# Performance work log

Measured on AMD Instinct MI355X. Metric: run time of the kernel, lower is better.

Reference implementation:

```python
import jax, jax.numpy as jnp
import numpy as np

E, H, F, N, B = 512, 8, 2048, 1024, 4
HD = E // H


def setup_inputs() -> dict:
    key = jax.random.key(0)
    ks = jax.random.split(key, 20)
    s = 0.02
    return {
        "node_inputs": jax.random.normal(ks[0], (N, B, E), jnp.float32),
        "parent_mask": jax.random.uniform(ks[1], (B, N, N), jnp.float32),
        "hidden": jax.random.bernoulli(ks[2], 0.5, (B, N, N)),
        "pad_mask": jax.random.bernoulli(ks[3], 0.1, (B, N)),
        "Wp": jax.random.normal(ks[4], (H, E), jnp.float32) * s,
        "bp": jnp.zeros((H,), jnp.float32),
        "Wc": jax.random.normal(ks[5], (H, E), jnp.float32) * s,
        "bc": jnp.zeros((H,), jnp.float32),
        "Wqkv": jax.random.normal(ks[6], (3 * E, E), jnp.float32) * s,
        "bqkv": jnp.zeros((3 * E,), jnp.float32),
        "Wo": jax.random.normal(ks[7], (E, E), jnp.float32) * s,
        "bo": jnp.zeros((E,), jnp.float32),
        "W1": jax.random.normal(ks[8], (F, E), jnp.float32) * s,
        "b1": jnp.zeros((F,), jnp.float32),
        "W2": jax.random.normal(ks[9], (E, F), jnp.float32) * s,
        "b2": jnp.zeros((E,), jnp.float32),
        "ln1_g": jnp.ones((E,), jnp.float32),
        "ln1_b": jnp.zeros((E,), jnp.float32),
        "ln2_g": jnp.ones((E,), jnp.float32),
        "ln2_b": jnp.zeros((E,), jnp.float32),
    }


def _layer_norm(x, g, b, eps=1e-5):
    m = jnp.mean(x, axis=-1, keepdims=True)
    v = jnp.mean((x - m) ** 2, axis=-1, keepdims=True)
    return (x - m) * jax.lax.rsqrt(v + eps) * g + b


def reference(node_inputs, parent_mask, hidden, pad_mask, Wp, bp, Wc, bc,
              Wqkv, bqkv, Wo, bo, W1, b1, W2, b2, ln1_g, ln1_b, ln2_g, ln2_b):
    x = node_inputs  # (N, B, E), seq-first like nn.TransformerEncoderLayer
    # parent/child per-head biases: Linear(E->H), permuted to (B, H, N)
    pbias = jnp.transpose(x @ Wp.T + bp, (1, 2, 0))
    cbias = jnp.transpose(x @ Wc.T + bc, (1, 2, 0))
    # additive attention bias (B, H, N, N)
    am = (jnp.swapaxes(parent_mask, 1, 2)[:, None] * pbias[..., None]
          + parent_mask[:, None] * cbias[..., None])
    am = jnp.where(hidden[:, None], -jnp.inf, am)
    # multi-head self-attention
    qkv = x @ Wqkv.T + bqkv  # (N, B, 3E)
    q, k, v = jnp.split(qkv, 3, axis=-1)

    def heads(t):  # (N, B, E) -> (B, H, N, HD)
        return jnp.transpose(t.reshape(N, B, H, HD), (1, 2, 0, 3))

    q, k, v = heads(q), heads(k), heads(v)
    scores = jnp.einsum("bhqd,bhkd->bhqk", q, k) / jnp.sqrt(jnp.float32(HD)) + am
    scores = jnp.where(pad_mask[:, None, None, :], -jnp.inf, scores)
    attn = jax.nn.softmax(scores, axis=-1)
    ctx = jnp.einsum("bhqk,bhkd->bhqd", attn, v)  # (B, H, N, HD)
    ctx = jnp.transpose(ctx, (2, 0, 1, 3)).reshape(N, B, E)
    attn_out = ctx @ Wo.T + bo
    # post-norm transformer encoder layer (dropout=0, relu activation)
    y = _layer_norm(x + attn_out, ln1_g, ln1_b)
    ff = jax.nn.relu(y @ W1.T + b1) @ W2.T + b2
    return _layer_norm(y + ff, ln2_g, ln2_b)
```

## Files before the change

kernel.cpp:

```cpp
#include <hip/hip_runtime.h>
#include <hip/hip_bf16.h>
#include <stdint.h>

using bf16 = __hip_bfloat16;

typedef __bf16 bf16x8 __attribute__((ext_vector_type(8)));
typedef float  f32x4  __attribute__((ext_vector_type(4)));

__device__ __forceinline__ float bflo(uint32_t u) { return __uint_as_float(u << 16); }
__device__ __forceinline__ float bfhi(uint32_t u) { return __uint_as_float(u & 0xffff0000u); }

__device__ __forceinline__ void load8(const bf16* p, float* f) {
  uint4 u = *(const uint4*)p;
  f[0] = bflo(u.x); f[1] = bfhi(u.x);
  f[2] = bflo(u.y); f[3] = bfhi(u.y);
  f[4] = bflo(u.z); f[5] = bfhi(u.z);
  f[6] = bflo(u.w); f[7] = bfhi(u.w);
}
__device__ __forceinline__ void load8(const float* p, float* f) {
  float4 a = *(const float4*)p, b = *(const float4*)(p + 4);
  f[0] = a.x; f[1] = a.y; f[2] = a.z; f[3] = a.w;
  f[4] = b.x; f[5] = b.y; f[6] = b.z; f[7] = b.w;
}
__device__ __forceinline__ void store1(float* o, float v) { *o = v; }
__device__ __forceinline__ void store1(bf16* o, float v) { *o = __float2bfloat16(v); }
__device__ __forceinline__ uint32_t bfbits(float x) {
  bf16 v = __float2bfloat16(x);
  return (uint32_t)*(uint16_t*)&v;
}

typedef const uint32_t __attribute__((address_space(1)))* gp_t;
typedef uint32_t __attribute__((address_space(3)))* lp_t;
__device__ __forceinline__ void gload16(const void* g, void* l) {
  __builtin_amdgcn_global_load_lds((gp_t)g, (lp_t)l, 16, 0, 0);
}

__global__ __launch_bounds__(256)
void prep_mask(const float* __restrict__ pm, const int* __restrict__ hid,
               const int* __restrict__ padm, uint32_t* __restrict__ mout,
               const float* __restrict__ x, const float* __restrict__ Wqkv,
               const float* __restrict__ Wo, const float* __restrict__ W1,
               const float* __restrict__ W2, bf16* __restrict__ xb,
               bf16* __restrict__ wq, bf16* __restrict__ wob,
               bf16* __restrict__ w1b, bf16* __restrict__ w2b,
               const float* __restrict__ bqkv, const float* __restrict__ bp,
               const float* __restrict__ bc, const float* __restrict__ Wp,
               const float* __restrict__ Wc, float* __restrict__ bias_ext)
{
  __shared__ float tileT[128][65];
  const int t = threadIdx.x;
  if (blockIdx.x < 512) {
    const int mb = blockIdx.x;
    const int k0 = (mb & 7) * 128, q0 = ((mb >> 3) & 15) * 64, b = mb >> 7;
    const size_t pb = (size_t)b << 20;
#pragma unroll
    for (int i = 0; i < 32; ++i) {
      int idx = t + i * 256;
      int r = idx >> 6, c = idx & 63;
      tileT[r][c] = pm[pb + (size_t)(k0 + r) * 1024 + q0 + c];
    }
    __syncthreads();
#pragma unroll
    for (int i = 0; i < 32; ++i) {
      int idx = t + i * 256;
      int q = idx >> 7, k = idx & 127;
      size_t src = pb + (size_t)(q0 + q) * 1024 + k0 + k;
      int msk = hid[src] | padm[b * 1024 + k0 + k];
      uint32_t u = 0xFFFFFFFFu;
      if (!msk) u = (bfbits(tileT[k][q]) << 16) | bfbits(pm[src]);
      mout[src] = u;
    }
    return;
  }
  const int blk = blockIdx.x - 512;
  if (blk < 2560) {
    size_t j = ((size_t)blk * 256 + t) * 8;
    const float* s; bf16* o; size_t off;
    if      (j < 2097152) { s = x;    o = xb;  off = j; }
    else if (j < 2883584) { s = Wqkv; o = wq;  off = j - 2097152; }
    else if (j < 3145728) { s = Wo;   o = wob; off = j - 2883584; }
    else if (j < 4194304) { s = W1;   o = w1b; off = j - 3145728; }
    else                  { s = W2;   o = w2b; off = j - 4194304; }
    float f[8];
    load8(s + off, f);
    uint4 u;
    u.x = (bfbits(f[1]) << 16) | bfbits(f[0]);
    u.y = (bfbits(f[3]) << 16) | bfbits(f[2]);
    u.z = (bfbits(f[5]) << 16) | bfbits(f[4]);
    u.w = (bfbits(f[7]) << 16) | bfbits(f[6]);
    *(uint4*)(o + off) = u;
  } else {
    int sb = blk - 2560;
    if (sb < 2) {
      int j = (sb * 256 + t) * 8;
      if (j < 4096) {
        float f[8]; load8(Wp + j, f);
#pragma unroll
        for (int i = 0; i < 8; ++i) wq[(size_t)1536 * 512 + j + i] = __float2bfloat16(f[i]);
      }
    } else if (sb < 4) {
      int j = ((sb - 2) * 256 + t) * 8;
      if (j < 4096) {
        float f[8]; load8(Wc + j, f);
#pragma unroll
        for (int i = 0; i < 8; ++i) wq[(size_t)1544 * 512 + j + i] = __float2bfloat16(f[i]);
      }
    } else {
      int j = t * 8;
#pragma unroll
      for (int i = 0; i < 8; ++i) {
        int cc = j + i;
        if (cc < 1664) {
          float v = 0.f;
          if (cc < 1536) v = bqkv[cc];
          else if (cc < 1544) v = bp[cc - 1536];
          else if (cc < 1552) v = bc[cc - 1544];
          bias_ext[cc] = v;
        }
      }
    }
  }
}

__global__ __launch_bounds__(256)
void qkv_gemm(const bf16* __restrict__ A, const bf16* __restrict__ W,
              const float* __restrict__ bias, bf16* __restrict__ outb,
              float* __restrict__ outf)
{
  __shared__ bf16 As[2][128 * 64];
  __shared__ bf16 Bs[2][128 * 64];
  const int t = threadIdx.x;
  const int lane = t & 63, wave = t >> 6;
  const int m0 = (blockIdx.x / 13) * 128, n0 = (blockIdx.x % 13) * 128;
  const int wr = wave >> 1, wc = wave & 1;
  const int frow = lane & 15, ksel = (lane >> 4) * 8;
  f32x4 acc[16] = {};
  const bf16* Ab = A + (size_t)m0 * 512;
  const bf16* Wb = W + (size_t)n0 * 512;

  const int ibs = wave * 64 + lane;
#define STAGE(buf, k0)                                                        \
  {                                                                           \
    _Pragma("unroll")                                                         \
    for (int i = 0; i < 4; ++i) {                                             \
      int idx = i * 256 + ibs;                                                \
      gload16(Ab + (size_t)(idx >> 3) * 512 + (k0) + (idx & 7) * 8,           \
              &As[buf][(i * 256 + wave * 64) * 8]);                           \
    }                                                                         \
    _Pragma("unroll")                                                         \
    for (int i = 0; i < 4; ++i) {                                             \
      int idx = i * 256 + ibs;                                                \
      gload16(Wb + (size_t)(idx >> 3) * 512 + (k0) + (idx & 7) * 8,           \
              &Bs[buf][(i * 256 + wave * 64) * 8]);                           \
    }                                                                         \
  }

  STAGE(0, 0);
  __syncthreads();
#pragma unroll
  for (int ks = 0; ks < 8; ++ks) {
    const int cur = ks & 1;
    if (ks < 7) STAGE(cur ^ 1, (ks + 1) * 64);
#pragma unroll
    for (int kk = 0; kk < 64; kk += 32) {
      bf16x8 af[4], bf_[4];
#pragma unroll
      for (int mt = 0; mt < 4; ++mt)
        af[mt] = *(const bf16x8*)(&As[cur][(wr * 64 + mt * 16 + frow) * 64 + kk + ksel]);
#pragma unroll
      for (int nt = 0; nt < 4; ++nt)
        bf_[nt] = *(const bf16x8*)(&Bs[cur][(wc * 64 + nt * 16 + frow) * 64 + kk + ksel]);
#pragma unroll
      for (int mt = 0; mt < 4; ++mt)
#pragma unroll
        for (int nt = 0; nt < 4; ++nt)
          acc[mt * 4 + nt] = __builtin_amdgcn_mfma_f32_16x16x32_bf16(
              af[mt], bf_[nt], acc[mt * 4 + nt], 0, 0, 0);
    }
    __syncthreads();
  }
#undef STAGE

  const int rb = (lane >> 4) * 4, cb = lane & 15;
#pragma unroll
  for (int mt = 0; mt < 4; ++mt)
#pragma unroll
    for (int nt = 0; nt < 4; ++nt) {
      f32x4 a = acc[mt * 4 + nt];
#pragma unroll
      for (int r = 0; r < 4; ++r) {
        int row = m0 + wr * 64 + mt * 16 + rb + r;
        int col = n0 + wc * 64 + nt * 16 + cb;
        if (col >= 1552) continue;
        float v = a[r] + bias[col];
        int n = row >> 2, b = row & 3;
        if (col >= 1536) {
          int j = col - 1536;
          int hh = j & 7;
          outf[(j < 8 ? 0 : 32768) + (b * 8 + hh) * 1024 + n] = v;
        } else {
          int which = col >> 9, hh = (col >> 6) & 7, d = col & 63;
          if (which == 0) v *= 0.125f;
          size_t idx;
          if (which == 2)
            idx = (((size_t)(64 + b * 8 + hh)) << 16) + (size_t)d * 1024 + n;
          else
            idx = (((size_t)(which * 32 + b * 8 + hh)) << 16) + (size_t)n * 64 + d;
          outb[idx] = __float2bfloat16(v);
        }
      }
    }
}

template<int MODE, int BN>
__global__ __launch_bounds__(256)
void gemm_bt(const bf16* __restrict__ A, const bf16* __restrict__ W,
             const float* __restrict__ bias, bf16* __restrict__ outb,
             float* __restrict__ outf, int M, int Nout, int K, int kLen)
{
  constexpr int NT = BN / 32;
  __shared__ bf16 As[128 * 64];
  __shared__ bf16 Bs[BN * 64];
  const int t = threadIdx.x, lane = t & 63, wave = t >> 6;
  const int m0 = blockIdx.y * 128, n0 = blockIdx.x * BN;
  const int kOff = blockIdx.z * kLen;
  if (MODE == 3) outf += (size_t)blockIdx.z * M * Nout;
  const int wr = wave >> 1, wc = wave & 1;
  const int frow = lane & 15, ksel = (lane >> 4) * 8;
  f32x4 acc[4 * NT] = {};
  const bf16* Ab = A + (size_t)m0 * K;
  const bf16* Wb = W + (size_t)n0 * K;

  for (int k0 = kOff; k0 < kOff + kLen; k0 += 64) {
    __syncthreads();
#pragma unroll
    for (int i = 0; i < 4; ++i) {
      int ib = i * 256 + wave * 64;
      int idx = ib + lane;
      gload16(Ab + (size_t)(idx >> 3) * K + k0 + (idx & 7) * 8, As + ib * 8);
    }
#pragma unroll
    for (int i = 0; i < BN / 32; ++i) {
      int ib = i * 256 + wave * 64;
      int idx = ib + lane;
      gload16(Wb + (size_t)(idx >> 3) * K + k0 + (idx & 7) * 8, Bs + ib * 8);
    }
    __syncthreads();
#pragma unroll
    for (int kk = 0; kk < 64; kk += 32) {
      bf16x8 af[4], bf_[NT];
#pragma unroll
      for (int mt = 0; mt < 4; ++mt)
        af[mt] = *(const bf16x8*)(As + (wr * 64 + mt * 16 + frow) * 64 + kk + ksel);
#pragma unroll
      for (int nt = 0; nt < NT; ++nt)
        bf_[nt] = *(const bf16x8*)(Bs + (wc * (BN / 2) + nt * 16 + frow) * 64 + kk + ksel);
#pragma unroll
      for (int mt = 0; mt < 4; ++mt)
#pragma unroll
        for (int nt = 0; nt < NT; ++nt)
          acc[mt * NT + nt] = __builtin_amdgcn_mfma_f32_16x16x32_bf16(
              af[mt], bf_[nt], acc[mt * NT + nt], 0, 0, 0);
    }
  }
  const int rb = (lane >> 4) * 4, cb = lane & 15;
#pragma unroll
  for (int mt = 0; mt < 4; ++mt)
#pragma unroll
    for (int nt = 0; nt < NT; ++nt) {
      f32x4 a = acc[mt * NT + nt];
#pragma unroll
      for (int r = 0; r < 4; ++r) {
        int row = m0 + wr * 64 + mt * 16 + rb + r;
        int col = n0 + wc * (BN / 2) + nt * 16 + cb;
        if (MODE == 3) {
          outf[(size_t)row * Nout + col] = a[r];
        } else {
          float v = a[r] + bias[col];
          if (MODE == 1) v = fmaxf(v, 0.f);
          outb[(size_t)row * Nout + col] = __float2bfloat16(v);
        }
      }
    }
}

__global__ __launch_bounds__(256, 2)
void attn_mfma(const bf16* __restrict__ qkv, const float* __restrict__ pbw,
               const float* __restrict__ cbw, const uint32_t* __restrict__ mpk,
               bf16* __restrict__ ctxo)
{
  __shared__ bf16 Kt[128 * 64];
  __shared__ bf16 Vt[64 * 128];
  __shared__ bf16 Ps[4][16][136];
  const int t = threadIdx.x, lane = t & 63, wave = t >> 6;
  const int g = lane >> 4, c = lane & 15;
  const int h = blockIdx.y, b = blockIdx.z;
  const int q0 = blockIdx.x * 64 + wave * 16;
  const size_t bh = (size_t)b * 8 + h;
  const bf16* Qp = qkv + (bh << 16);
  const bf16* Kp = qkv + ((32 + bh) << 16);
  const bf16* Vg = qkv + ((64 + bh) << 16);

  bf16x8 qa0 = *(const bf16x8*)(Qp + (size_t)(q0 + c) * 64 + g * 8);
  bf16x8 qa1 = *(const bf16x8*)(Qp + (size_t)(q0 + c) * 64 + 32 + g * 8);

  const float pbq = pbw[bh * 1024 + q0 + c];
  const float cbq = cbw[bh * 1024 + q0 + c];
  const uint32_t* mrp = mpk + (((size_t)b * 1024 + q0 + c) << 10);

  f32x4 oacc[4] = {{0,0,0,0},{0,0,0,0},{0,0,0,0},{0,0,0,0}};
  float m = -1e30f, l = 0.f;

  for (int kt = 0; kt < 8; ++kt) {
    const int k0 = kt * 128;
    __syncthreads();
#pragma unroll
    for (int i = 0; i < 4; ++i) {
      int ib = i * 256 + wave * 64;
      int idx = ib + lane;
      int r = idx >> 3, p = idx & 7;
      gload16(Kp + (size_t)(k0 + r) * 64 + ((p ^ (r & 7)) * 8), Kt + ib * 8);
    }
#pragma unroll
    for (int i = 0; i < 4; ++i) {
      int ib = i * 256 + wave * 64;
      int idx = ib + lane;
      int d = idx >> 4, p = idx & 15;
      gload16(Vg + (size_t)d * 1024 + k0 + ((p ^ (d & 15)) * 8), Vt + ib * 8);
    }
    uint4 mu[8];
#pragma unroll
    for (int nt = 0; nt < 8; ++nt)
      mu[nt] = *(const uint4*)(mrp + k0 + nt * 16 + 4 * g);
    __syncthreads();
    f32x4 sacc[8];
#pragma unroll
    for (int nt = 0; nt < 8; ++nt) {
      f32x4 z = {0.f,0.f,0.f,0.f};
      int r = nt * 16 + c;
      bf16x8 k0f = *(const bf16x8*)(Kt + r * 64 + (( g      ^ (c & 7)) * 8));
      bf16x8 k1f = *(const bf16x8*)(Kt + r * 64 + (((4 + g) ^ (c & 7)) * 8));
      z = __builtin_amdgcn_mfma_f32_16x16x32_bf16(k0f, qa0, z, 0, 0, 0);
      z = __builtin_amdgcn_mfma_f32_16x16x32_bf16(k1f, qa1, z, 0, 0, 0);
      sacc[nt] = z;
    }
    float mx = -1e30f;
#pragma unroll
    for (int nt = 0; nt < 8; ++nt) {
      uint32_t uu[4] = {mu[nt].x, mu[nt].y, mu[nt].z, mu[nt].w};
#pragma unroll
      for (int r = 0; r < 4; ++r) {
        float s = sacc[nt][r] + bfhi(uu[r]) * pbq + bflo(uu[r]) * cbq;
        s = (uu[r] == 0xFFFFFFFFu) ? -1e30f : s;
        sacc[nt][r] = s;
        mx = fmaxf(mx, s);
      }
    }
    mx = fmaxf(mx, __shfl_xor(mx, 16));
    mx = fmaxf(mx, __shfl_xor(mx, 32));
    const float newm = fmaxf(m, mx);
    const float al = __expf(m - newm);
    float ps = 0.f;
#pragma unroll
    for (int nt = 0; nt < 8; ++nt) {
      float p0 = (sacc[nt][0] <= -1e29f) ? 0.f : __expf(sacc[nt][0] - newm);
      float p1 = (sacc[nt][1] <= -1e29f) ? 0.f : __expf(sacc[nt][1] - newm);
      float p2 = (sacc[nt][2] <= -1e29f) ? 0.f : __expf(sacc[nt][2] - newm);
      float p3 = (sacc[nt][3] <= -1e29f) ? 0.f : __expf(sacc[nt][3] - newm);
      ps += (p0 + p1) + (p2 + p3);
      uint2 w;
      w.x = (bfbits(p1) << 16) | bfbits(p0);
      w.y = (bfbits(p3) << 16) | bfbits(p2);
      *(uint2*)&Ps[wave][c][nt * 16 + 4 * g] = w;
    }
    ps += __shfl_xor(ps, 16);
    ps += __shfl_xor(ps, 32);
    l = l * al + ps;
    m = newm;
#pragma unroll
    for (int dt = 0; dt < 4; ++dt) {
      oacc[dt][0] *= al; oacc[dt][1] *= al;
      oacc[dt][2] *= al; oacc[dt][3] *= al;
    }
#pragma unroll
    for (int dt = 0; dt < 4; ++dt) {
      int row = dt * 16 + c;
#pragma unroll
      for (int kc = 0; kc < 4; ++kc) {
        bf16x8 vf = *(const bf16x8*)(Vt + row * 128 + (((kc * 4 + g) ^ c) * 8));
        bf16x8 pf = *(const bf16x8*)&Ps[wave][c][kc * 32 + g * 8];
        oacc[dt] = __builtin_amdgcn_mfma_f32_16x16x32_bf16(vf, pf, oacc[dt], 0, 0, 0);
      }
    }
  }
  const int qg = q0 + c;
  const float inv = (l > 0.f) ? 1.f / l : 0.f;
  bf16* out = ctxo + ((size_t)qg * 4 + b) * 512 + h * 64;
#pragma unroll
  for (int dt = 0; dt < 4; ++dt) {
    uint2 w;
    w.x = (bfbits(oacc[dt][1] * inv) << 16) | bfbits(oacc[dt][0] * inv);
    w.y = (bfbits(oacc[dt][3] * inv) << 16) | bfbits(oacc[dt][2] * inv);
    *(uint2*)(out + dt * 16 + 4 * g) = w;
  }
}

template<typename TA, typename TO>
__global__ __launch_bounds__(256)
void ln_res2(const TA* __restrict__ a, const float* __restrict__ p0,
             const float* __restrict__ p1, const float* __restrict__ bias,
             const float* __restrict__ g, const float* __restrict__ be,
             TO* __restrict__ out)
{
  const int wave = threadIdx.x >> 6, lane = threadIdx.x & 63;
  const int m = blockIdx.x * 4 + wave;
  const size_t base = (size_t)m * 512 + lane * 8;
  float va[8], f0[8], f1[8], bb[8];
  load8(a + base, va);
  load8(p0 + base, f0);
  load8(p1 + base, f1);
  load8(bias + lane * 8, bb);
  float v[8], s = 0.f;
#pragma unroll
  for (int j = 0; j < 8; ++j) { v[j] = va[j] + f0[j] + f1[j] + bb[j]; s += v[j]; }
#pragma unroll
  for (int off = 32; off; off >>= 1) s += __shfl_xor(s, off);
  const float mean = s * (1.f / 512.f);
  float q = 0.f;
#pragma unroll
  for (int j = 0; j < 8; ++j) { float d = v[j] - mean; q += d * d; }
#pragma unroll
  for (int off = 32; off; off >>= 1) q += __shfl_xor(q, off);
  const float rs = rsqrtf(q * (1.f / 512.f) + 1e-5f);
  float gv[8], bv[8];
  load8(g + lane * 8, gv);
  load8(be + lane * 8, bv);
#pragma unroll
  for (int j = 0; j < 8; ++j)
    store1(out + base + j, (v[j] - mean) * rs * gv[j] + bv[j]);
}

extern "C" void kernel_launch(void* const* d_in, const int* in_sizes, int n_in,
                              void* d_out, int out_size, void* d_ws, size_t ws_size,
                              hipStream_t stream)
{
  (void)in_sizes; (void)n_in; (void)out_size; (void)ws_size;
  const float* x    = (const float*)d_in[0];
  const float* pm   = (const float*)d_in[1];
  const int*   hid  = (const int*)d_in[2];
  const int*   padm = (const int*)d_in[3];
  const float* Wp   = (const float*)d_in[4];
  const float* bp   = (const float*)d_in[5];
  const float* Wc   = (const float*)d_in[6];
  const float* bc   = (const float*)d_in[7];
  const float* Wqkv = (const float*)d_in[8];
  const float* bqkv = (const float*)d_in[9];
  const float* Wo   = (const float*)d_in[10];
  const float* bo   = (const float*)d_in[11];
  const float* W1   = (const float*)d_in[12];
  const float* b1   = (const float*)d_in[13];
  const float* W2   = (const float*)d_in[14];
  const float* b2   = (const float*)d_in[15];
  const float* g1   = (const float*)d_in[16];
  const float* be1  = (const float*)d_in[17];
  const float* g2   = (const float*)d_in[18];
  const float* be2  = (const float*)d_in[19];

  char* ws = (char*)d_ws;
  bf16*     qkvb  = (bf16*)    (ws);
  float*    pbo   = (float*)   (ws + 12582912);
  float*    cbo   = (float*)   (ws + 12713984);
  uint32_t* mpk   = (uint32_t*)(ws + 12845056);
  bf16*     ctx   = (bf16*)    (ws + 29622272);
  float*    part  = (float*)   (ws);
  bf16*     ff1   = (bf16*)    (ws + 16777216);
  bf16*     y     = (bf16*)    (ws + 33816576);
  bf16*     xb    = (bf16*)    (ws + 38010880);
  bf16*     wqkvb = (bf16*)    (ws + 42205184);
  bf16*     wob   = (bf16*)    (ws + 43909120);
  bf16*     w1b   = (bf16*)    (ws + 44433408);
  bf16*     w2b   = (bf16*)    (ws + 46530560);
  float*    bext  = (float*)   (ws + 48627712);
  float*    part1 = part + (size_t)4096 * 512;

  prep_mask<<<3077, 256, 0, stream>>>(pm, hid, padm, mpk,
                                      x, Wqkv, Wo, W1, W2, xb, wqkvb, wob, w1b, w2b,
                                      bqkv, bp, bc, Wp, Wc, bext);
  qkv_gemm<<<416, 256, 0, stream>>>(xb, wqkvb, bext, qkvb, pbo);
  attn_mfma<<<dim3(16, 8, 4), 256, 0, stream>>>(qkvb, pbo, cbo, mpk, ctx);
  gemm_bt<3, 64><<<dim3(8, 32, 2), 256, 0, stream>>>(ctx, wob, nullptr, nullptr, part, 4096, 512, 512, 256);
  ln_res2<float, bf16><<<1024, 256, 0, stream>>>(x, part, part1, bo, g1, be1, y);
  gemm_bt<1, 128><<<dim3(16, 32), 256, 0, stream>>>(y, w1b, b1, ff1, nullptr, 4096, 2048, 512, 512);
  gemm_bt<3, 64><<<dim3(8, 32, 2), 256, 0, stream>>>(ff1, w2b, nullptr, nullptr, part, 4096, 512, 2048, 1024);
  ln_res2<bf16, float><<<1024, 256, 0, stream>>>(y, part, part1, b2, g2, be2, (float*)d_out);
}
```

Baseline: 258.7 us.

## Double-buffer K tiles and mask prefetch in attention, read V from global

The attention kernel now double-buffers K tiles in shared memory and prefetches the next tile's packed mask words into registers, so loads for the next key block overlap compute on the current one. V fragments are read directly from global memory instead of being staged through LDS, which halves the shared-memory staging but puts strided global loads on the PV MFMA path. The prep kernel stores the transposed mask tile as bf16 bits to shrink shared memory, and each weight-conversion block now handles five chunks, cutting the grid from 3077 to 1029 blocks. The per-iteration barrier moves to the end of the loop body.

Result: slower. 286.0 us (+10.5%).

```diff
diff --git a/kernel.cpp b/kernel.cpp
--- a/kernel.cpp
+++ b/kernel.cpp
@@ -47,7 +47,7 @@
                const float* __restrict__ bc, const float* __restrict__ Wp,
                const float* __restrict__ Wc, float* __restrict__ bias_ext)
 {
-  __shared__ float tileT[128][65];
+  __shared__ ushort tileT[128][70];
   const int t = threadIdx.x;
   if (blockIdx.x < 512) {
     const int mb = blockIdx.x;
@@ -57,7 +57,7 @@
     for (int i = 0; i < 32; ++i) {
       int idx = t + i * 256;
       int r = idx >> 6, c = idx & 63;
-      tileT[r][c] = pm[pb + (size_t)(k0 + r) * 1024 + q0 + c];
+      tileT[r][c] = (ushort)bfbits(pm[pb + (size_t)(k0 + r) * 1024 + q0 + c]);
     }
     __syncthreads();
 #pragma unroll
@@ -67,30 +67,38 @@
       size_t src = pb + (size_t)(q0 + q) * 1024 + k0 + k;
       int msk = hid[src] | padm[b * 1024 + k0 + k];
       uint32_t u = 0xFFFFFFFFu;
-      if (!msk) u = (bfbits(tileT[k][q]) << 16) | bfbits(pm[src]);
+      if (!msk) u = ((uint32_t)tileT[k][q] << 16) | bfbits(pm[src]);
       mout[src] = u;
     }
     return;
   }
   const int blk = blockIdx.x - 512;
-  if (blk < 2560) {
-    size_t j = ((size_t)blk * 256 + t) * 8;
-    const float* s; bf16* o; size_t off;
-    if      (j < 2097152) { s = x;    o = xb;  off = j; }
-    else if (j < 2883584) { s = Wqkv; o = wq;  off = j - 2097152; }
-    else if (j < 3145728) { s = Wo;   o = wob; off = j - 2883584; }
-    else if (j < 4194304) { s = W1;   o = w1b; off = j - 3145728; }
-    else                  { s = W2;   o = w2b; off = j - 4194304; }
-    float f[8];
-    load8(s + off, f);
-    uint4 u;
-    u.x = (bfbits(f[1]) << 16) | bfbits(f[0]);
-    u.y = (bfbits(f[3]) << 16) | bfbits(f[2]);
-    u.z = (bfbits(f[5]) << 16) | bfbits(f[4]);
-    u.w = (bfbits(f[7]) << 16) | bfbits(f[6]);
-    *(uint4*)(o + off) = u;
+  if (blk < 512) {
+    float f[5][8];
+    bf16* op[5];
+#pragma unroll
+    for (int u = 0; u < 5; ++u) {
+      size_t j = ((size_t)(blk + u * 512) * 256 + t) * 8;
+      const float* s; bf16* o; size_t off;
+      if      (j < 2097152) { s = x;    o = xb;  off = j; }
+      else if (j < 2883584) { s = Wqkv; o = wq;  off = j - 2097152; }
+      else if (j < 3145728) { s = Wo;   o = wob; off = j - 2883584; }
+      else if (j < 4194304) { s = W1;   o = w1b; off = j - 3145728; }
+      else                  { s = W2;   o = w2b; off = j - 4194304; }
+      load8(s + off, f[u]);
+      op[u] = o + off;
+    }
+#pragma unroll
+    for (int u = 0; u < 5; ++u) {
+      uint4 uu;
+      uu.x = (bfbits(f[u][1]) << 16) | bfbits(f[u][0]);
+      uu.y = (bfbits(f[u][3]) << 16) | bfbits(f[u][2]);
+      uu.z = (bfbits(f[u][5]) << 16) | bfbits(f[u][4]);
+      uu.w = (bfbits(f[u][7]) << 16) | bfbits(f[u][6]);
+      *(uint4*)op[u] = uu;
+    }
   } else {
-    int sb = blk - 2560;
+    int sb = blk - 512;
     if (sb < 2) {
       int j = (sb * 256 + t) * 8;
       if (j < 4096) {
@@ -289,8 +297,7 @@
                const float* __restrict__ cbw, const uint32_t* __restrict__ mpk,
                bf16* __restrict__ ctxo)
 {
-  __shared__ bf16 Kt[128 * 64];
-  __shared__ bf16 Vt[64 * 128];
+  __shared__ bf16 Kt[2][128 * 64];
   __shared__ bf16 Ps[4][16][136];
   const int t = threadIdx.x, lane = t & 63, wave = t >> 6;
   const int g = lane >> 4, c = lane & 15;
@@ -311,35 +318,44 @@
   f32x4 oacc[4] = {{0,0,0,0},{0,0,0,0},{0,0,0,0},{0,0,0,0}};
   float m = -1e30f, l = 0.f;
 
+#define STAGE_K(buf, kk0)                                                     \
+  {                                                                           \
+    _Pragma("unroll")                                                         \
+    for (int i = 0; i < 4; ++i) {                                             \
+      int ib = i * 256 + wave * 64;                                           \
+      int idx = ib + lane;                                                    \
+      int r = idx >> 3, p = idx & 7;                                          \
+      gload16(Kp + (size_t)((kk0) + r) * 64 + ((p ^ (r & 7)) * 8),            \
+              &Kt[buf][ib * 8]);                                              \
+    }                                                                         \
+  }
+
+  STAGE_K(0, 0);
+  uint4 mun[8];
+#pragma unroll
+  for (int nt = 0; nt < 8; ++nt)
+    mun[nt] = *(const uint4*)(mrp + nt * 16 + 4 * g);
+  __syncthreads();
+
   for (int kt = 0; kt < 8; ++kt) {
+    const int cur = kt & 1;
     const int k0 = kt * 128;
-    __syncthreads();
-#pragma unroll
-    for (int i = 0; i < 4; ++i) {
-      int ib = i * 256 + wave * 64;
-      int idx = ib + lane;
-      int r = idx >> 3, p = idx & 7;
-      gload16(Kp + (size_t)(k0 + r) * 64 + ((p ^ (r & 7)) * 8), Kt + ib * 8);
-    }
-#pragma unroll
-    for (int i = 0; i < 4; ++i) {
-      int ib = i * 256 + wave * 64;
-      int idx = ib + lane;
-      int d = idx >> 4, p = idx & 15;
-      gload16(Vg + (size_t)d * 1024 + k0 + ((p ^ (d & 15)) * 8), Vt + ib * 8);
-    }
+    if (kt < 7) STAGE_K(cur ^ 1, k0 + 128);
     uint4 mu[8];
 #pragma unroll
-    for (int nt = 0; nt < 8; ++nt)
-      mu[nt] = *(const uint4*)(mrp + k0 + nt * 16 + 4 * g);
-    __syncthreads();
+    for (int nt = 0; nt < 8; ++nt) mu[nt] = mun[nt];
+    if (kt < 7) {
+#pragma unroll
+      for (int nt = 0; nt < 8; ++nt)
+        mun[nt] = *(const uint4*)(mrp + k0 + 128 + nt * 16 + 4 * g);
+    }
     f32x4 sacc[8];
 #pragma unroll
     for (int nt = 0; nt < 8; ++nt) {
       f32x4 z = {0.f,0.f,0.f,0.f};
       int r = nt * 16 + c;
-      bf16x8 k0f = *(const bf16x8*)(Kt + r * 64 + (( g      ^ (c & 7)) * 8));
-      bf16x8 k1f = *(const bf16x8*)(Kt + r * 64 + (((4 + g) ^ (c & 7)) * 8));
+      bf16x8 k0f = *(const bf16x8*)(&Kt[cur][r * 64 + (( g      ^ (c & 7)) * 8)]);
+      bf16x8 k1f = *(const bf16x8*)(&Kt[cur][r * 64 + (((4 + g) ^ (c & 7)) * 8)]);
       z = __builtin_amdgcn_mfma_f32_16x16x32_bf16(k0f, qa0, z, 0, 0, 0);
       z = __builtin_amdgcn_mfma_f32_16x16x32_bf16(k1f, qa1, z, 0, 0, 0);
       sacc[nt] = z;
@@ -387,12 +403,15 @@
       int row = dt * 16 + c;
 #pragma unroll
       for (int kc = 0; kc < 4; ++kc) {
-        bf16x8 vf = *(const bf16x8*)(Vt + row * 128 + (((kc * 4 + g) ^ c) * 8));
+        bf16x8 vf = *(const bf16x8*)(Vg + (size_t)row * 1024 + k0 + (kc * 4 + g) * 8);
         bf16x8 pf = *(const bf16x8*)&Ps[wave][c][kc * 32 + g * 8];
         oacc[dt] = __builtin_amdgcn_mfma_f32_16x16x32_bf16(vf, pf, oacc[dt], 0, 0, 0);
       }
     }
-  }
+    __syncthreads();
+  }
+#undef STAGE_K
+
   const int qg = q0 + c;
   const float inv = (l > 0.f) ? 1.f / l : 0.f;
   bf16* out = ctxo + ((size_t)qg * 4 + b) * 512 + h * 64;
@@ -483,7 +502,7 @@
   float*    bext  = (float*)   (ws + 48627712);
   float*    part1 = part + (size_t)4096 * 512;
 
-  prep_mask<<<3077, 256, 0, stream>>>(pm, hid, padm, mpk,
+  prep_mask<<<1029, 256, 0, stream>>>(pm, hid, padm, mpk,
                                       x, Wqkv, Wo, W1, W2, xb, wqkvb, wob, w1b, w2b,
                                       bqkv, bp, bc, Wp, Wc, bext);
   qkv_gemm<<<416, 256, 0, stream>>>(xb, wqkvb, bext, qkvb, pbo);
```
